# Kernel optimization log

Hardware: AMD Instinct MI355X
Metric: run time of the kernel (lower is better)

Reference implementation:

```python
import jax, jax.numpy as jnp
import numpy as np

B, D_MODEL, N, H = 4, 256, 2048, 4
HEAD_DIM = D_MODEL // H  # 64


def _rotate_half(x):
    # x: [..., d] with d even; pairs (x1, x2) -> (-x2, x1)
    x = x.reshape(x.shape[:-1] + (x.shape[-1] // 2, 2))
    x1, x2 = x[..., 0], x[..., 1]
    return jnp.stack((-x2, x1), axis=-1).reshape(x.shape[:-2] + (-1,))


def _apply_rope(freqs, t):
    # freqs: [2, n, d] (cos, sin); t: [b, h, n, d]
    return t * freqs[0] + _rotate_half(t) * freqs[1]


def setup_inputs() -> dict:
    key = jax.random.key(0)
    ks = jax.random.split(key, 12)
    s = 0.02
    inp = {
        "query": jax.random.normal(ks[0], (B, D_MODEL, N), jnp.float32),
        "key": jax.random.normal(ks[1], (B, D_MODEL, N), jnp.float32),
        "value": jax.random.normal(ks[2], (B, D_MODEL, N), jnp.float32),
        "encoding": jax.random.normal(ks[3], (2, N, HEAD_DIM), jnp.float32),
        "Wq": jax.random.normal(ks[4], (D_MODEL, D_MODEL), jnp.float32) * s,
        "bq": jnp.zeros((D_MODEL,), jnp.float32),
        "Wk": jax.random.normal(ks[5], (D_MODEL, D_MODEL), jnp.float32) * s,
        "bk": jnp.zeros((D_MODEL,), jnp.float32),
        "Wv": jax.random.normal(ks[6], (D_MODEL, D_MODEL), jnp.float32) * s,
        "bv": jnp.zeros((D_MODEL,), jnp.float32),
        "Wm": jax.random.normal(ks[7], (D_MODEL, D_MODEL), jnp.float32) * s,
        "bm": jnp.zeros((D_MODEL,), jnp.float32),
    }
    return inp


def _proj(W, b, x):
    # 1x1 Conv1d == channel matmul: x [b, c_in, n] -> [b, c_out, n]
    return jnp.einsum('oi,bin->bon', W, x) + b[None, :, None]


def reference(query, key, value, encoding, Wq, bq, Wk, bk, Wv, bv, Wm, bm):
    b = query.shape[0]
    # project and split channels into (head_dim, heads): [b, d, h, n]
    q = _proj(Wq, bq, query).reshape(b, HEAD_DIM, H, -1)
    k = _proj(Wk, bk, key).reshape(b, HEAD_DIM, H, -1)
    v = _proj(Wv, bv, value).reshape(b, HEAD_DIM, H, -1)
    # RoPE on [b, h, n, d] layout
    q = jnp.transpose(_apply_rope(encoding, jnp.transpose(q, (0, 2, 3, 1))), (0, 3, 1, 2))
    k = jnp.transpose(_apply_rope(encoding, jnp.transpose(k, (0, 2, 3, 1))), (0, 3, 1, 2))
    # attention: scores [b, h, n, m]
    scores = jnp.einsum('bdhn,bdhm->bhnm', q, k) / jnp.sqrt(jnp.float32(HEAD_DIM))
    prob = jax.nn.softmax(scores, axis=-1)
    x = jnp.einsum('bhnm,bdhm->bdhn', prob, v)
    x = x.reshape(b, HEAD_DIM * H, -1)
    return _proj(Wm, bm, x)
```

## Files before the change

kernel.cpp:

```cpp
#include <hip/hip_runtime.h>
#include <stdint.h>

#define NSEQ 2048

typedef __attribute__((ext_vector_type(4))) float f32x4;
typedef __attribute__((ext_vector_type(8))) short s16x8;
typedef _Float16 f16x8 __attribute__((ext_vector_type(8)));

#define OFF_XT  0u
#define OFF_XA  0u
#define OFF_PO  4194304u
#define OFF_W   12582912u
#define OFF_QR  13107200u
#define OFF_KR  17301504u
#define OFF_VT  21495808u
#define OFF_M   25690112u
#define OFF_L   25952256u

__device__ __forceinline__ short f2h(float f) {
  _Float16 h = (_Float16)f;
  return __builtin_bit_cast(short, h);
}
__device__ __forceinline__ float h2f(short s) {
  return (float)__builtin_bit_cast(_Float16, s);
}
__device__ __forceinline__ int swz128(int row, int slot) {
  return row * 128 + ((slot ^ (row & 7)) << 4);
}
#define MFMA(a, b, c) __builtin_amdgcn_mfma_f32_16x16x32_f16(a, b, c, 0, 0, 0)

__global__ void k_convw(const float* __restrict__ Wq, const float* __restrict__ Wk,
                        const float* __restrict__ Wv, const float* __restrict__ Wm,
                        char* __restrict__ ws) {
  int o = blockIdx.x, which = blockIdx.y, i = threadIdx.x;
  const float* src = which == 0 ? Wq : which == 1 ? Wk : which == 2 ? Wv : Wm;
  short* dst = (short*)(ws + OFF_W) + which * 65536;
  float val = (which < 3) ? src[o * 256 + i] : src[o * 256 + ((i & 63) << 2) + (i >> 6)];
  dst[o * 256 + i] = f2h(val);
}

__global__ __launch_bounds__(256) void k_trans(const float* __restrict__ q,
    const float* __restrict__ k, const float* __restrict__ v, char* __restrict__ ws) {
  int tensor = blockIdx.z >> 2, b = blockIdx.z & 3;
  const float* src = tensor == 0 ? q : (tensor == 1 ? k : v);
  short* dst = (short*)(ws + OFF_XT) + (tensor * 4 + b) * 524288;
  int n0 = blockIdx.x * 64, i0 = blockIdx.y * 64;
  __shared__ float tile[64][65];
  int t = threadIdx.x;
  int nl = t & 63, ib = (t >> 6) * 16;
#pragma unroll
  for (int r = 0; r < 16; ++r)
    tile[ib + r][nl] = src[(b * 256 + i0 + ib + r) * 2048 + n0 + nl];
  __syncthreads();
  int nr = t >> 2, ic = (t & 3) * 16;
  short tmp[16];
#pragma unroll
  for (int j = 0; j < 16; ++j) tmp[j] = f2h(tile[ic + j][nr]);
  short* dp = &dst[(n0 + nr) * 256 + i0 + ic];
  *(s16x8*)dp = *(const s16x8*)&tmp[0];
  *(s16x8*)(dp + 8) = *(const s16x8*)&tmp[8];
}

__device__ __forceinline__ void gemm128(const short* __restrict__ W, const short* __restrict__ X,
                                        int o0, int n0, short* As, short* Bs, f32x4 acc[4][4]) {
  int t = threadIdx.x;
  int lane = t & 63, g = lane >> 4, c = lane & 15, wave = t >> 6;
  int wo = (wave >> 1) * 64, wn = (wave & 1) * 64;
  int row = t >> 1, half = t & 1;
  for (int kk = 0; kk < 4; ++kk) {
    __syncthreads();
    int koff = kk * 64 + half * 32;
    const short* wsrc = &W[(o0 + row) * 256 + koff];
    const short* xsrc = &X[(n0 + row) * 256 + koff];
#pragma unroll
    for (int q4 = 0; q4 < 4; ++q4) {
      *(s16x8*)((char*)As + swz128(row, half * 4 + q4)) = *(const s16x8*)(wsrc + q4 * 8);
      *(s16x8*)((char*)Bs + swz128(row, half * 4 + q4)) = *(const s16x8*)(xsrc + q4 * 8);
    }
    __syncthreads();
#pragma unroll
    for (int ks = 0; ks < 2; ++ks) {
      f16x8 af[4], bfr[4];
#pragma unroll
      for (int f = 0; f < 4; ++f) {
        af[f]  = *(const f16x8*)((char*)As + swz128(wo + f * 16 + c, ks * 4 + g));
        bfr[f] = *(const f16x8*)((char*)Bs + swz128(wn + f * 16 + c, ks * 4 + g));
      }
#pragma unroll
      for (int i = 0; i < 4; ++i)
#pragma unroll
        for (int j = 0; j < 4; ++j)
          acc[i][j] = MFMA(af[i], bfr[j], acc[i][j]);
    }
  }
}

__global__ __launch_bounds__(256) void k_proj(const float* __restrict__ enc,
    const float* __restrict__ bq, const float* __restrict__ bk, const float* __restrict__ bv,
    char* __restrict__ ws) {
  int proj = blockIdx.z >> 2, b = blockIdx.z & 3;
  const short* W = (const short*)(ws + OFF_W) + proj * 65536;
  const short* X = (const short*)(ws + OFF_XT) + (proj * 4 + b) * 524288;
  int o0 = blockIdx.y * 128, n0 = blockIdx.x * 128;
  __shared__ short As[128 * 64], Bs[128 * 64];
  f32x4 acc[4][4] = {};
  gemm128(W, X, o0, n0, As, Bs, acc);
  int t = threadIdx.x, lane = t & 63, g = lane >> 4, c = lane & 15, wave = t >> 6;
  int wo = (wave >> 1) * 64, wn = (wave & 1) * 64;
  const float* bias = proj == 0 ? bq : (proj == 1 ? bk : bv);
  if (proj < 2) {
    short* dst0 = (short*)(ws + (proj == 0 ? OFF_QR : OFF_KR));
    float scale = proj == 0 ? 0.18033688f : 1.0f;
    float sgn = (g & 1) ? 1.0f : -1.0f;
#pragma unroll
    for (int i = 0; i < 4; ++i) {
      int ob = o0 + wo + i * 16 + g * 4;
      int d = ob >> 2;
#pragma unroll
      for (int j = 0; j < 4; ++j) {
        int n = n0 + wn + j * 16 + c;
        float cv = enc[n * 64 + d], sv = enc[131072 + n * 64 + d];
#pragma unroll
        for (int r = 0; r < 4; ++r) {
          float val = acc[i][j][r] + bias[ob + r];
          float par = __shfl_xor(val, 16, 64);
          float res = (val * cv + sgn * par * sv) * scale;
          dst0[((b * 4 + r) * 2048 + n) * 64 + d] = f2h(res);
        }
      }
    }
  } else {
    short* dst = (short*)(ws + OFF_VT);
#pragma unroll
    for (int i = 0; i < 4; ++i) {
      int ob = o0 + wo + i * 16 + g * 4;
      int d = ob >> 2;
#pragma unroll
      for (int j = 0; j < 4; ++j) {
        int n = n0 + wn + j * 16 + c;
#pragma unroll
        for (int r = 0; r < 4; ++r) {
          float val = acc[i][j][r] + bias[ob + r];
          dst[((b * 4 + r) * 64 + d) * 2048 + n] = f2h(val);
        }
      }
    }
  }
}

__global__ __launch_bounds__(256, 4) void k_attn(char* __restrict__ ws) {
  int bh = blockIdx.y, ms = blockIdx.z;
  int t = threadIdx.x, wave = t >> 6, lane = t & 63, g = lane >> 4, c = lane & 15;
  int nw = blockIdx.x * 64 + wave * 16;
  const short* Q = (const short*)(ws + OFF_QR) + bh * 131072;
  const short* K = (const short*)(ws + OFF_KR) + bh * 131072;
  const short* V = (const short*)(ws + OFF_VT) + bh * 131072;
  __shared__ short Ks[64 * 64], Vs[64 * 64], Ps[4][16 * 64];
  char* Pb = (char*)Ps[wave];
  f16x8 qf0 = *(const f16x8*)&Q[(nw + c) * 64 + g * 8];
  f16x8 qf1 = *(const f16x8*)&Q[(nw + c) * 64 + 32 + g * 8];
  f32x4 po[4] = {};
  float mrun = -1e30f, lrun = 0.f;
  int sr = t >> 3, sl = t & 7;
  const int mb = ms * 1024;
  int bsrc = g * 16 + g * 4;

  s16x8 RA[4], RB[4];
  auto LD = [&](int m0, s16x8* R) {
    R[0] = *(const s16x8*)&K[(m0 + sr) * 64 + sl * 8];
    R[1] = *(const s16x8*)&K[(m0 + sr + 32) * 64 + sl * 8];
    R[2] = *(const s16x8*)&V[sr * 2048 + m0 + sl * 8];
    R[3] = *(const s16x8*)&V[(sr + 32) * 2048 + m0 + sl * 8];
  };
  auto ST = [&](const s16x8* R) {
    *(s16x8*)((char*)Ks + swz128(sr, sl))      = R[0];
    *(s16x8*)((char*)Ks + swz128(sr + 32, sl)) = R[1];
    *(s16x8*)((char*)Vs + swz128(sr, sl))      = R[2];
    *(s16x8*)((char*)Vs + swz128(sr + 32, sl)) = R[3];
  };
  auto COMPUTE = [&]() {
    f32x4 s[4] = {};
    __builtin_amdgcn_s_setprio(1);
#pragma unroll
    for (int fj = 0; fj < 4; ++fj) {
      f16x8 k0 = *(const f16x8*)((char*)Ks + swz128(fj * 16 + c, g));
      f16x8 k1 = *(const f16x8*)((char*)Ks + swz128(fj * 16 + c, 4 + g));
      s[fj] = MFMA(k0, qf0, s[fj]);
      s[fj] = MFMA(k1, qf1, s[fj]);
    }
    __builtin_amdgcn_s_setprio(0);
    float t0 = fmaxf(fmaxf(s[0][0], s[0][1]), fmaxf(s[0][2], s[0][3]));
    float t1 = fmaxf(fmaxf(s[1][0], s[1][1]), fmaxf(s[1][2], s[1][3]));
    float t2 = fmaxf(fmaxf(s[2][0], s[2][1]), fmaxf(s[2][2], s[2][3]));
    float t3 = fmaxf(fmaxf(s[3][0], s[3][1]), fmaxf(s[3][2], s[3][3]));
    float rmax = fmaxf(fmaxf(t0, t1), fmaxf(t2, t3));
    rmax = fmaxf(rmax, __shfl_xor(rmax, 16, 64));
    rmax = fmaxf(rmax, __shfl_xor(rmax, 32, 64));
    if (__any(rmax > mrun + 11.5f)) {
      float nm = fmaxf(mrun, rmax);
      float corr = exp2f(mrun - nm);
      mrun = nm;
      lrun *= corr;
#pragma unroll
      for (int r = 0; r < 4; ++r) {
        float corr_r = __shfl(corr, bsrc + r, 64);
#pragma unroll
        for (int fd = 0; fd < 4; ++fd) po[fd][r] *= corr_r;
      }
    }
    float p[4][4], rs = 0.f;
#pragma unroll
    for (int fj = 0; fj < 4; ++fj) {
      f32x4 pv;
#pragma unroll
      for (int r = 0; r < 4; ++r) {
        pv[r] = exp2f(s[fj][r] - mrun);
        p[fj][r] = pv[r];
      }
      rs += (pv[0] + pv[1]) + (pv[2] + pv[3]);
    }
    rs += __shfl_xor(rs, 16, 64);
    rs += __shfl_xor(rs, 32, 64);
    lrun += rs;
#pragma unroll
    for (int fj = 0; fj < 4; ++fj)
#pragma unroll
      for (int r = 0; r < 4; ++r) {
        int mm = fj * 16 + g * 4 + r;
        *(short*)(Pb + swz128(c, mm >> 3) + (mm & 7) * 2) = f2h(p[fj][r]);
      }
    asm volatile("s_waitcnt lgkmcnt(0)" ::: "memory");
    __builtin_amdgcn_sched_barrier(0);
    f16x8 pa0 = *(const f16x8*)(Pb + swz128(c, g));
    f16x8 pa1 = *(const f16x8*)(Pb + swz128(c, 4 + g));
    __builtin_amdgcn_s_setprio(1);
#pragma unroll
    for (int fd = 0; fd < 4; ++fd) {
      int dd = fd * 16 + c;
      f16x8 vb0 = *(const f16x8*)((char*)Vs + swz128(dd, g));
      f16x8 vb1 = *(const f16x8*)((char*)Vs + swz128(dd, 4 + g));
      po[fd] = MFMA(pa0, vb0, po[fd]);
      po[fd] = MFMA(pa1, vb1, po[fd]);
    }
    __builtin_amdgcn_s_setprio(0);
  };

  LD(mb, RA);
  for (int tt = 0; tt < 16; tt += 2) {
    __syncthreads();
    ST(RA);
    LD(mb + (tt + 1) * 64, RB);
    __syncthreads();
    COMPUTE();
    __syncthreads();
    ST(RB);
    if (tt + 2 < 16) LD(mb + (tt + 2) * 64, RA);
    __syncthreads();
    COMPUTE();
  }

  short* PO = (short*)(ws + OFF_PO);
  float* Mm = (float*)(ws + OFF_M);
  float* Ll = (float*)(ws + OFF_L);
  int base = (ms * 16 + bh) * 2048;
  float li[4];
#pragma unroll
  for (int r = 0; r < 4; ++r) li[r] = 1.0f / __shfl(lrun, bsrc + r, 64);
#pragma unroll
  for (int fd = 0; fd < 4; ++fd) {
    int d = fd * 16 + c;
#pragma unroll
    for (int r = 0; r < 4; ++r) {
      int n = nw + g * 4 + r;
      PO[(base + n) * 64 + d] = f2h(po[fd][r] * li[r]);
    }
  }
  if (g == 0) {
    Mm[base + nw + c] = mrun;
    Ll[base + nw + c] = lrun;
  }
}

__global__ __launch_bounds__(256) void k_comb(char* __restrict__ ws) {
  int t = threadIdx.x;
  int row = blockIdx.x * 32 + (t >> 3);
  int bh = row >> 11, n = row & 2047;
  int dc = (t & 7) * 8;
  const short* PO = (const short*)(ws + OFF_PO);
  const float* Mm = (const float*)(ws + OFF_M);
  const float* Ll = (const float*)(ws + OFF_L);
  float m1 = Mm[row], m2 = Mm[32768 + row];
  float l1 = Ll[row], l2 = Ll[32768 + row];
  float M = fmaxf(m1, m2);
  float w1 = l1 * exp2f(m1 - M), w2 = l2 * exp2f(m2 - M);
  float inv = 1.f / (w1 + w2);
  float a1 = w1 * inv, a2 = w2 * inv;
  s16x8 o1 = *(const s16x8*)&PO[row * 64 + dc];
  s16x8 o2 = *(const s16x8*)&PO[(32768 + row) * 64 + dc];
  short res[8];
#pragma unroll
  for (int j = 0; j < 8; ++j) res[j] = f2h(a1 * h2f(o1[j]) + a2 * h2f(o2[j]));
  short* XA = (short*)(ws + OFF_XA);
  int b = bh >> 2, h = bh & 3;
  *(s16x8*)&XA[(b * 2048 + n) * 256 + h * 64 + dc] = *(const s16x8*)res;
}

__global__ __launch_bounds__(256) void k_final(const float* __restrict__ bm,
    float* __restrict__ out, char* __restrict__ ws) {
  int b = blockIdx.z;
  const short* W = (const short*)(ws + OFF_W) + 3 * 65536;
  const short* X = (const short*)(ws + OFF_XA) + b * 524288;
  int o0 = blockIdx.y * 128, n0 = blockIdx.x * 128;
  __shared__ short As[128 * 64], Bs[128 * 64];
  f32x4 acc[4][4] = {};
  gemm128(W, X, o0, n0, As, Bs, acc);
  int t = threadIdx.x, lane = t & 63, g = lane >> 4, c = lane & 15, wave = t >> 6;
  int wo = (wave >> 1) * 64, wn = (wave & 1) * 64;
#pragma unroll
  for (int i = 0; i < 4; ++i) {
    int ob = o0 + wo + i * 16 + g * 4;
#pragma unroll
    for (int j = 0; j < 4; ++j) {
      int n = n0 + wn + j * 16 + c;
#pragma unroll
      for (int r = 0; r < 4; ++r)
        out[(b * 256 + ob + r) * 2048 + n] = acc[i][j][r] + bm[ob + r];
    }
  }
}

extern "C" void kernel_launch(void* const* d_in, const int* in_sizes, int n_in,
                              void* d_out, int out_size, void* d_ws, size_t ws_size,
                              hipStream_t stream) {
  (void)in_sizes; (void)n_in; (void)out_size; (void)ws_size;
  const float* q   = (const float*)d_in[0];
  const float* k   = (const float*)d_in[1];
  const float* v   = (const float*)d_in[2];
  const float* enc = (const float*)d_in[3];
  const float* Wq  = (const float*)d_in[4];
  const float* bq  = (const float*)d_in[5];
  const float* Wk  = (const float*)d_in[6];
  const float* bk  = (const float*)d_in[7];
  const float* Wv  = (const float*)d_in[8];
  const float* bv  = (const float*)d_in[9];
  const float* Wm  = (const float*)d_in[10];
  const float* bm  = (const float*)d_in[11];
  char* ws = (char*)d_ws;
  float* out = (float*)d_out;
  hipLaunchKernelGGL(k_convw, dim3(256, 4), dim3(256), 0, stream, Wq, Wk, Wv, Wm, ws);
  hipLaunchKernelGGL(k_trans, dim3(32, 4, 12), dim3(256), 0, stream, q, k, v, ws);
  hipLaunchKernelGGL(k_proj, dim3(16, 2, 12), dim3(256), 0, stream, enc, bq, bk, bv, ws);
  hipLaunchKernelGGL(k_attn, dim3(32, 16, 2), dim3(256), 0, stream, ws);
  hipLaunchKernelGGL(k_comb, dim3(1024), dim3(256), 0, stream, ws);
  hipLaunchKernelGGL(k_final, dim3(16, 2, 4), dim3(256), 0, stream, bm, out, ws);
}
```

Measured before the change: 161.5 us.

## Fuse weight conversion and split-KV combine into GEMMs, raise KV split to four

Drops the separate weight-conversion kernel: the projection and output GEMMs now read fp32 weights directly and convert them to fp16 while filling shared memory. The split-KV combine kernel is folded into the final projection, which merges four partial attention outputs per row while loading its B tile. The attention KV split goes from 2 to 4 so more blocks run concurrently, and the GEMM tiles shrink from 128 to 64 to give more blocks. This removes two launches and one intermediate round trip through memory. In exchange the fp32 weights are converted redundantly in every block, the final GEMM reads Wm with a strided gather, and more partial outputs have to be written and read back.

```diff
diff --git a/kernel.cpp b/kernel.cpp
--- a/kernel.cpp
+++ b/kernel.cpp
@@ -8,14 +8,12 @@
 typedef _Float16 f16x8 __attribute__((ext_vector_type(8)));
 
 #define OFF_XT  0u
-#define OFF_XA  0u
-#define OFF_PO  4194304u
-#define OFF_W   12582912u
-#define OFF_QR  13107200u
-#define OFF_KR  17301504u
-#define OFF_VT  21495808u
-#define OFF_M   25690112u
-#define OFF_L   25952256u
+#define OFF_PO  0u
+#define OFF_M   16777216u
+#define OFF_L   17301504u
+#define OFF_QR  17825792u
+#define OFF_KR  22020096u
+#define OFF_VT  26214400u
 
 __device__ __forceinline__ short f2h(float f) {
   _Float16 h = (_Float16)f;
@@ -28,16 +26,6 @@
   return row * 128 + ((slot ^ (row & 7)) << 4);
 }
 #define MFMA(a, b, c) __builtin_amdgcn_mfma_f32_16x16x32_f16(a, b, c, 0, 0, 0)
-
-__global__ void k_convw(const float* __restrict__ Wq, const float* __restrict__ Wk,
-                        const float* __restrict__ Wv, const float* __restrict__ Wm,
-                        char* __restrict__ ws) {
-  int o = blockIdx.x, which = blockIdx.y, i = threadIdx.x;
-  const float* src = which == 0 ? Wq : which == 1 ? Wk : which == 2 ? Wv : Wm;
-  short* dst = (short*)(ws + OFF_W) + which * 65536;
-  float val = (which < 3) ? src[o * 256 + i] : src[o * 256 + ((i & 63) << 2) + (i >> 6)];
-  dst[o * 256 + i] = f2h(val);
-}
 
 __global__ __launch_bounds__(256) void k_trans(const float* __restrict__ q,
     const float* __restrict__ k, const float* __restrict__ v, char* __restrict__ ws) {
@@ -61,64 +49,63 @@
   *(s16x8*)(dp + 8) = *(const s16x8*)&tmp[8];
 }
 
-__device__ __forceinline__ void gemm128(const short* __restrict__ W, const short* __restrict__ X,
-                                        int o0, int n0, short* As, short* Bs, f32x4 acc[4][4]) {
-  int t = threadIdx.x;
-  int lane = t & 63, g = lane >> 4, c = lane & 15, wave = t >> 6;
-  int wo = (wave >> 1) * 64, wn = (wave & 1) * 64;
-  int row = t >> 1, half = t & 1;
+__global__ __launch_bounds__(256) void k_proj(const float* __restrict__ Wq,
+    const float* __restrict__ Wk, const float* __restrict__ Wv,
+    const float* __restrict__ enc, const float* __restrict__ bq,
+    const float* __restrict__ bk, const float* __restrict__ bv, char* __restrict__ ws) {
+  int proj = blockIdx.z >> 2, b = blockIdx.z & 3;
+  const float* W = proj == 0 ? Wq : (proj == 1 ? Wk : Wv);
+  const short* X = (const short*)(ws + OFF_XT) + (proj * 4 + b) * 524288;
+  int o0 = blockIdx.y * 64, n0 = blockIdx.x * 64;
+  __shared__ short As[64 * 64], Bs[64 * 64];
+  int t = threadIdx.x, lane = t & 63, g = lane >> 4, c = lane & 15, wave = t >> 6;
+  int wr = wave >> 1, wc = wave & 1;
+  int row = t >> 2, seg = t & 3;
+  f32x4 acc[2][2] = {};
   for (int kk = 0; kk < 4; ++kk) {
     __syncthreads();
-    int koff = kk * 64 + half * 32;
-    const short* wsrc = &W[(o0 + row) * 256 + koff];
+    int koff = kk * 64;
+    const float* wsrc = &W[(o0 + row) * 256 + koff + seg * 16];
+    short ha[16];
+#pragma unroll
+    for (int q4 = 0; q4 < 4; ++q4) {
+      f32x4 wv4 = *(const f32x4*)(wsrc + q4 * 4);
+#pragma unroll
+      for (int j = 0; j < 4; ++j) ha[q4 * 4 + j] = f2h(wv4[j]);
+    }
+    *(s16x8*)((char*)As + swz128(row, seg * 2))     = *(const s16x8*)&ha[0];
+    *(s16x8*)((char*)As + swz128(row, seg * 2 + 1)) = *(const s16x8*)&ha[8];
     const short* xsrc = &X[(n0 + row) * 256 + koff];
-#pragma unroll
-    for (int q4 = 0; q4 < 4; ++q4) {
-      *(s16x8*)((char*)As + swz128(row, half * 4 + q4)) = *(const s16x8*)(wsrc + q4 * 8);
-      *(s16x8*)((char*)Bs + swz128(row, half * 4 + q4)) = *(const s16x8*)(xsrc + q4 * 8);
-    }
+    *(s16x8*)((char*)Bs + swz128(row, seg))     = *(const s16x8*)(xsrc + seg * 8);
+    *(s16x8*)((char*)Bs + swz128(row, 4 + seg)) = *(const s16x8*)(xsrc + 32 + seg * 8);
     __syncthreads();
 #pragma unroll
     for (int ks = 0; ks < 2; ++ks) {
-      f16x8 af[4], bfr[4];
-#pragma unroll
-      for (int f = 0; f < 4; ++f) {
-        af[f]  = *(const f16x8*)((char*)As + swz128(wo + f * 16 + c, ks * 4 + g));
-        bfr[f] = *(const f16x8*)((char*)Bs + swz128(wn + f * 16 + c, ks * 4 + g));
-      }
-#pragma unroll
-      for (int i = 0; i < 4; ++i)
-#pragma unroll
-        for (int j = 0; j < 4; ++j)
+      f16x8 af[2], bfr[2];
+#pragma unroll
+      for (int f = 0; f < 2; ++f) {
+        af[f]  = *(const f16x8*)((char*)As + swz128(wr * 32 + f * 16 + c, ks * 4 + g));
+        bfr[f] = *(const f16x8*)((char*)Bs + swz128(wc * 32 + f * 16 + c, ks * 4 + g));
+      }
+#pragma unroll
+      for (int i = 0; i < 2; ++i)
+#pragma unroll
+        for (int j = 0; j < 2; ++j)
           acc[i][j] = MFMA(af[i], bfr[j], acc[i][j]);
     }
   }
-}
-
-__global__ __launch_bounds__(256) void k_proj(const float* __restrict__ enc,
-    const float* __restrict__ bq, const float* __restrict__ bk, const float* __restrict__ bv,
-    char* __restrict__ ws) {
-  int proj = blockIdx.z >> 2, b = blockIdx.z & 3;
-  const short* W = (const short*)(ws + OFF_W) + proj * 65536;
-  const short* X = (const short*)(ws + OFF_XT) + (proj * 4 + b) * 524288;
-  int o0 = blockIdx.y * 128, n0 = blockIdx.x * 128;
-  __shared__ short As[128 * 64], Bs[128 * 64];
-  f32x4 acc[4][4] = {};
-  gemm128(W, X, o0, n0, As, Bs, acc);
-  int t = threadIdx.x, lane = t & 63, g = lane >> 4, c = lane & 15, wave = t >> 6;
-  int wo = (wave >> 1) * 64, wn = (wave & 1) * 64;
   const float* bias = proj == 0 ? bq : (proj == 1 ? bk : bv);
   if (proj < 2) {
     short* dst0 = (short*)(ws + (proj == 0 ? OFF_QR : OFF_KR));
     float scale = proj == 0 ? 0.18033688f : 1.0f;
     float sgn = (g & 1) ? 1.0f : -1.0f;
 #pragma unroll
-    for (int i = 0; i < 4; ++i) {
-      int ob = o0 + wo + i * 16 + g * 4;
+    for (int i = 0; i < 2; ++i) {
+      int ob = o0 + wr * 32 + i * 16 + g * 4;
       int d = ob >> 2;
 #pragma unroll
-      for (int j = 0; j < 4; ++j) {
-        int n = n0 + wn + j * 16 + c;
+      for (int j = 0; j < 2; ++j) {
+        int n = n0 + wc * 32 + j * 16 + c;
         float cv = enc[n * 64 + d], sv = enc[131072 + n * 64 + d];
 #pragma unroll
         for (int r = 0; r < 4; ++r) {
@@ -132,12 +119,12 @@
   } else {
     short* dst = (short*)(ws + OFF_VT);
 #pragma unroll
-    for (int i = 0; i < 4; ++i) {
-      int ob = o0 + wo + i * 16 + g * 4;
+    for (int i = 0; i < 2; ++i) {
+      int ob = o0 + wr * 32 + i * 16 + g * 4;
       int d = ob >> 2;
 #pragma unroll
-      for (int j = 0; j < 4; ++j) {
-        int n = n0 + wn + j * 16 + c;
+      for (int j = 0; j < 2; ++j) {
+        int n = n0 + wc * 32 + j * 16 + c;
 #pragma unroll
         for (int r = 0; r < 4; ++r) {
           float val = acc[i][j][r] + bias[ob + r];
@@ -162,7 +149,7 @@
   f32x4 po[4] = {};
   float mrun = -1e30f, lrun = 0.f;
   int sr = t >> 3, sl = t & 7;
-  const int mb = ms * 1024;
+  const int mb = ms * 512;
   int bsrc = g * 16 + g * 4;
 
   s16x8 RA[4], RB[4];
@@ -246,7 +233,7 @@
   };
 
   LD(mb, RA);
-  for (int tt = 0; tt < 16; tt += 2) {
+  for (int tt = 0; tt < 8; tt += 2) {
     __syncthreads();
     ST(RA);
     LD(mb + (tt + 1) * 64, RB);
@@ -254,7 +241,7 @@
     COMPUTE();
     __syncthreads();
     ST(RB);
-    if (tt + 2 < 16) LD(mb + (tt + 2) * 64, RA);
+    if (tt + 2 < 8) LD(mb + (tt + 2) * 64, RA);
     __syncthreads();
     COMPUTE();
   }
@@ -281,47 +268,80 @@
   }
 }
 
-__global__ __launch_bounds__(256) void k_comb(char* __restrict__ ws) {
-  int t = threadIdx.x;
-  int row = blockIdx.x * 32 + (t >> 3);
-  int bh = row >> 11, n = row & 2047;
-  int dc = (t & 7) * 8;
+__global__ __launch_bounds__(256) void k_final(const float* __restrict__ Wm,
+    const float* __restrict__ bm, float* __restrict__ out, char* __restrict__ ws) {
+  int b = blockIdx.z;
+  int o0 = blockIdx.y * 64, n0 = blockIdx.x * 64;
   const short* PO = (const short*)(ws + OFF_PO);
   const float* Mm = (const float*)(ws + OFF_M);
   const float* Ll = (const float*)(ws + OFF_L);
-  float m1 = Mm[row], m2 = Mm[32768 + row];
-  float l1 = Ll[row], l2 = Ll[32768 + row];
-  float M = fmaxf(m1, m2);
-  float w1 = l1 * exp2f(m1 - M), w2 = l2 * exp2f(m2 - M);
-  float inv = 1.f / (w1 + w2);
-  float a1 = w1 * inv, a2 = w2 * inv;
-  s16x8 o1 = *(const s16x8*)&PO[row * 64 + dc];
-  s16x8 o2 = *(const s16x8*)&PO[(32768 + row) * 64 + dc];
-  short res[8];
-#pragma unroll
-  for (int j = 0; j < 8; ++j) res[j] = f2h(a1 * h2f(o1[j]) + a2 * h2f(o2[j]));
-  short* XA = (short*)(ws + OFF_XA);
-  int b = bh >> 2, h = bh & 3;
-  *(s16x8*)&XA[(b * 2048 + n) * 256 + h * 64 + dc] = *(const s16x8*)res;
-}
-
-__global__ __launch_bounds__(256) void k_final(const float* __restrict__ bm,
-    float* __restrict__ out, char* __restrict__ ws) {
-  int b = blockIdx.z;
-  const short* W = (const short*)(ws + OFF_W) + 3 * 65536;
-  const short* X = (const short*)(ws + OFF_XA) + b * 524288;
-  int o0 = blockIdx.y * 128, n0 = blockIdx.x * 128;
-  __shared__ short As[128 * 64], Bs[128 * 64];
-  f32x4 acc[4][4] = {};
-  gemm128(W, X, o0, n0, As, Bs, acc);
+  __shared__ short As[64 * 64], Bs[64 * 64];
   int t = threadIdx.x, lane = t & 63, g = lane >> 4, c = lane & 15, wave = t >> 6;
-  int wo = (wave >> 1) * 64, wn = (wave & 1) * 64;
-#pragma unroll
-  for (int i = 0; i < 4; ++i) {
-    int ob = o0 + wo + i * 16 + g * 4;
-#pragma unroll
-    for (int j = 0; j < 4; ++j) {
-      int n = n0 + wn + j * 16 + c;
+  int wr = wave >> 1, wc = wave & 1;
+  int row = t >> 2, seg = t & 3;
+  f32x4 acc[2][2] = {};
+  for (int kk = 0; kk < 4; ++kk) {
+    __syncthreads();
+    short ha[16];
+#pragma unroll
+    for (int j = 0; j < 16; ++j)
+      ha[j] = f2h(Wm[(o0 + row) * 256 + (seg * 16 + j) * 4 + kk]);
+    *(s16x8*)((char*)As + swz128(row, seg * 2))     = *(const s16x8*)&ha[0];
+    *(s16x8*)((char*)As + swz128(row, seg * 2 + 1)) = *(const s16x8*)&ha[8];
+    int bh = b * 4 + kk;
+    int nr = n0 + row;
+    float m0 = Mm[(0 * 16 + bh) * 2048 + nr], l0 = Ll[(0 * 16 + bh) * 2048 + nr];
+    float m1 = Mm[(1 * 16 + bh) * 2048 + nr], l1 = Ll[(1 * 16 + bh) * 2048 + nr];
+    float m2 = Mm[(2 * 16 + bh) * 2048 + nr], l2 = Ll[(2 * 16 + bh) * 2048 + nr];
+    float m3 = Mm[(3 * 16 + bh) * 2048 + nr], l3 = Ll[(3 * 16 + bh) * 2048 + nr];
+    float M = fmaxf(fmaxf(m0, m1), fmaxf(m2, m3));
+    float w0 = l0 * exp2f(m0 - M), w1 = l1 * exp2f(m1 - M);
+    float w2 = l2 * exp2f(m2 - M), w3 = l3 * exp2f(m3 - M);
+    float inv = 1.f / (w0 + w1 + w2 + w3);
+    w0 *= inv; w1 *= inv; w2 *= inv; w3 *= inv;
+    float cb[16];
+    {
+      const short* p0 = &PO[((0 * 16 + bh) * 2048 + nr) * 64 + seg * 16];
+      const short* p1 = &PO[((1 * 16 + bh) * 2048 + nr) * 64 + seg * 16];
+      const short* p2 = &PO[((2 * 16 + bh) * 2048 + nr) * 64 + seg * 16];
+      const short* p3 = &PO[((3 * 16 + bh) * 2048 + nr) * 64 + seg * 16];
+      s16x8 a0 = *(const s16x8*)p0, a1 = *(const s16x8*)(p0 + 8);
+      s16x8 b0 = *(const s16x8*)p1, b1 = *(const s16x8*)(p1 + 8);
+      s16x8 c0 = *(const s16x8*)p2, c1 = *(const s16x8*)(p2 + 8);
+      s16x8 d0 = *(const s16x8*)p3, d1 = *(const s16x8*)(p3 + 8);
+#pragma unroll
+      for (int j = 0; j < 8; ++j) {
+        cb[j]     = w0 * h2f(a0[j]) + w1 * h2f(b0[j]) + w2 * h2f(c0[j]) + w3 * h2f(d0[j]);
+        cb[j + 8] = w0 * h2f(a1[j]) + w1 * h2f(b1[j]) + w2 * h2f(c1[j]) + w3 * h2f(d1[j]);
+      }
+    }
+    short hb[16];
+#pragma unroll
+    for (int j = 0; j < 16; ++j) hb[j] = f2h(cb[j]);
+    *(s16x8*)((char*)Bs + swz128(row, seg * 2))     = *(const s16x8*)&hb[0];
+    *(s16x8*)((char*)Bs + swz128(row, seg * 2 + 1)) = *(const s16x8*)&hb[8];
+    __syncthreads();
+#pragma unroll
+    for (int ks = 0; ks < 2; ++ks) {
+      f16x8 af[2], bfr[2];
+#pragma unroll
+      for (int f = 0; f < 2; ++f) {
+        af[f]  = *(const f16x8*)((char*)As + swz128(wr * 32 + f * 16 + c, ks * 4 + g));
+        bfr[f] = *(const f16x8*)((char*)Bs + swz128(wc * 32 + f * 16 + c, ks * 4 + g));
+      }
+#pragma unroll
+      for (int i = 0; i < 2; ++i)
+#pragma unroll
+        for (int j = 0; j < 2; ++j)
+          acc[i][j] = MFMA(af[i], bfr[j], acc[i][j]);
+    }
+  }
+#pragma unroll
+  for (int i = 0; i < 2; ++i) {
+    int ob = o0 + wr * 32 + i * 16 + g * 4;
+#pragma unroll
+    for (int j = 0; j < 2; ++j) {
+      int n = n0 + wc * 32 + j * 16 + c;
 #pragma unroll
       for (int r = 0; r < 4; ++r)
         out[(b * 256 + ob + r) * 2048 + n] = acc[i][j][r] + bm[ob + r];
@@ -347,10 +367,8 @@
   const float* bm  = (const float*)d_in[11];
   char* ws = (char*)d_ws;
   float* out = (float*)d_out;
-  hipLaunchKernelGGL(k_convw, dim3(256, 4), dim3(256), 0, stream, Wq, Wk, Wv, Wm, ws);
   hipLaunchKernelGGL(k_trans, dim3(32, 4, 12), dim3(256), 0, stream, q, k, v, ws);
-  hipLaunchKernelGGL(k_proj, dim3(16, 2, 12), dim3(256), 0, stream, enc, bq, bk, bv, ws);
-  hipLaunchKernelGGL(k_attn, dim3(32, 16, 2), dim3(256), 0, stream, ws);
-  hipLaunchKernelGGL(k_comb, dim3(1024), dim3(256), 0, stream, ws);
-  hipLaunchKernelGGL(k_final, dim3(16, 2, 4), dim3(256), 0, stream, bm, out, ws);
-}
+  hipLaunchKernelGGL(k_proj, dim3(32, 4, 12), dim3(256), 0, stream, Wq, Wk, Wv, enc, bq, bk, bv, ws);
+  hipLaunchKernelGGL(k_attn, dim3(32, 16, 4), dim3(256), 0, stream, ws);
+  hipLaunchKernelGGL(k_final, dim3(32, 4, 4), dim3(256), 0, stream, Wm, bm, out, ws);
+}
```

Result: no change. 161.1 us (-0.2%).
